# Kernel tuning notes

Hardware: AMD Instinct MI355X
Metric: run time of the kernel (lower is better)

The kernel has to match this reference:

```python
import jax, jax.numpy as jnp
import numpy as np
import math

B, C, H, W = 16, 512, 32, 32
HEADS = 8
HD = C // HEADS            # 64 head_dim
NFREQ = HD // 4            # 16 (head_dim % 4 == 0)
MAX_FREQ = 128.0
T = H * W                  # 1024 tokens


def _make_so2_mat():
    # make_2dcoord: meshgrid('ij') of arange(H), arange(W) -> [H, W, 2]
    xg, yg = np.meshgrid(np.arange(H, dtype=np.float32), np.arange(W, dtype=np.float32), indexing='ij')
    coord = np.stack([xg, yg], -1)                                   # [H, W, 2]
    freqs = np.exp(np.linspace(0.0, math.log(MAX_FREQ), NFREQ)).astype(np.float32)  # [NFREQ]
    th = coord[..., None, :] * freqs[None, None, :, None]            # [H, W, NFREQ, 2]
    c, s = np.cos(th), np.sin(th)
    # rotation matrices [[c, -s], [s, c]] -> [H, W, NFREQ, 2(dim), 2, 2]
    mat = np.stack([np.stack([c, -s], -1), np.stack([s, c], -1)], -2)
    mat = mat.reshape(H * W, NFREQ * 2, 2, 2)                        # flatten(2,3) then flatten(0,1)
    return jnp.asarray(mat[:, : HD // 2])                            # [T, HD//2, 2, 2]


def setup_inputs() -> dict:
    key = jax.random.key(0)
    ks = jax.random.split(key, 5)
    mat = _make_so2_mat()
    return {
        'x': jax.random.normal(ks[0], (B, C, H, W), dtype=jnp.float32),
        'w_qkv': jax.random.normal(ks[1], (3 * C, C), dtype=jnp.float32) * 0.02,
        'b_qkv': jax.random.normal(ks[2], (3 * C,), dtype=jnp.float32) * 0.02,
        'w_o': jax.random.normal(ks[3], (C, C), dtype=jnp.float32) * 0.02,
        'b_o': jax.random.normal(ks[4], (C,), dtype=jnp.float32) * 0.02,
        'mat_q': mat,
        'mat_k': mat,
        'mat_v': mat,
        'mat_o': jnp.swapaxes(mat, -2, -1),
    }


def _rep_mul(rep, t):
    # rep: [T, HD//2, 2, 2]; t: [B, nh, T, HD] -> per-pair 2x2 rotation
    tb = t.reshape(B, HEADS, T, HD // 2, 2)
    return jnp.einsum('tfij,bntfj->bntfi', rep, tb).reshape(B, HEADS, T, HD)


def _split_heads(t):
    # 'b (c nh) h w -> b nh (h w) c' (c outer, nh inner in channel dim)
    return t.reshape(B, HD, HEADS, T).transpose(0, 2, 3, 1)


def reference(x, w_qkv, b_qkv, w_o, b_o, mat_q, mat_k, mat_v, mat_o):
    # 1x1 conv QKV projection == channel GEMM
    qkv = jnp.einsum('bchw,oc->bohw', x, w_qkv) + b_qkv[None, :, None, None]
    q, k, v = jnp.split(qkv, 3, axis=1)
    q, k, v = map(_split_heads, (q, k, v))                 # [B, nh, T, HD]
    q = _rep_mul(mat_q, q)
    k = _rep_mul(mat_k, k)
    v = _rep_mul(mat_v, v)
    scale = 1.0 / math.sqrt(HD)
    attn = jax.nn.softmax(jnp.einsum('bntd,bnsd->bnts', q, k) * scale, axis=-1)
    o = jnp.einsum('bnts,bnsd->bntd', attn, v)             # [B, nh, T, HD]
    o = _rep_mul(mat_o, o)
    # 'b nh (h w) c -> b (c nh) h w'
    o = o.reshape(B, HEADS, H, W, HD).transpose(0, 4, 1, 2, 3).reshape(B, C, H, W)
    return jnp.einsum('bchw,oc->bohw', o, w_o) + b_o[None, :, None, None]
```

## Files before the change

### kernel.cpp

```cpp
#include <hip/hip_runtime.h>


typedef __bf16 bf16x8 __attribute__((ext_vector_type(8)));
typedef __bf16 bf16x4 __attribute__((ext_vector_type(4)));
typedef float  f32x4  __attribute__((ext_vector_type(4)));

__device__ __forceinline__ f32x4 mfma16(bf16x8 a, bf16x8 b, f32x4 c) {
    return __builtin_amdgcn_mfma_f32_16x16x32_bf16(a, b, c, 0, 0, 0);
}

__device__ __forceinline__ void async16(const void* g, void* l) {
    __builtin_amdgcn_global_load_lds(
        (const __attribute__((address_space(1))) void*)g,
        (__attribute__((address_space(3))) void*)l, 16, 0, 0);
}

__global__ void k_convert_w(const float* __restrict__ wq, const float* __restrict__ wo,
                            __bf16* __restrict__ wqb, __bf16* __restrict__ wob) {
    int i = blockIdx.x * 256 + threadIdx.x;
    if (i < 3 * 512 * 512) wqb[i] = (__bf16)wq[i];
    if (i < 512 * 512) {
        int o = i >> 9, k2 = i & 511;
        int nh = k2 >> 6, hd = k2 & 63;
        wob[i] = (__bf16)wo[o * 512 + hd * 8 + nh];
    }
}

__global__ void k_transpose_x(const float* __restrict__ x, __bf16* __restrict__ xt) {
    __shared__ float tile[32][33];
    const int b  = blockIdx.z;
    const int c0 = blockIdx.y * 32;
    const int t0 = blockIdx.x * 32;
    const int tx = threadIdx.x, ty = threadIdx.y;
    const float* xp = x + ((size_t)b * 512 + c0) * 1024 + t0;
#pragma unroll
    for (int j = 0; j < 4; j++)
        tile[ty + j * 8][tx] = xp[(ty + j * 8) * 1024 + tx];
    __syncthreads();
    __bf16* xo = xt + ((size_t)b * 1024 + t0) * 512 + c0;
#pragma unroll
    for (int j = 0; j < 4; j++)
        xo[(ty + j * 8) * 512 + tx] = (__bf16)tile[tx][ty + j * 8];
}

__global__ __launch_bounds__(256) void k_gemm_qkv(
        const __bf16* __restrict__ A, const __bf16* __restrict__ W,
        const float* __restrict__ bias,
        const float* __restrict__ matq, const float* __restrict__ matk,
        const float* __restrict__ matv,
        __bf16* __restrict__ qd, __bf16* __restrict__ kd, __bf16* __restrict__ vtd)
{
    __shared__ __bf16 As[128][64];
    __shared__ __bf16 Bs[128][64];
    const int tid = threadIdx.x;
    const int m0 = blockIdx.x * 128;
    const int jb = blockIdx.y;
    const int part = jb >> 2;
    const int nh_base = (jb & 3) * 2;
    const int lane = tid & 63, w = tid >> 6;
    const int ln = lane & 15, quad = lane >> 4;
    const int wr = w >> 1, wc = w & 1;

    const int srow = lane >> 3;
    const int scol = (((lane & 7) ^ srow) * 8);

    const __bf16* arow[4];
    const __bf16* brow[4];
#pragma unroll
    for (int jj = 0; jj < 4; jj++) {
        int rr = w * 32 + jj * 8 + srow;
        arow[jj] = &A[(size_t)(m0 + rr) * 512 + scol];
        int o = part * 512 + (rr & 63) * 8 + nh_base + (rr >> 6);
        brow[jj] = &W[(size_t)o * 512 + scol];
    }

    f32x4 acc[4][4] = {};

    for (int k0 = 0; k0 < 512; k0 += 64) {
#pragma unroll
        for (int jj = 0; jj < 4; jj++)
            async16(arow[jj] + k0, &As[w * 32 + jj * 8][0]);
#pragma unroll
        for (int jj = 0; jj < 4; jj++)
            async16(brow[jj] + k0, &Bs[w * 32 + jj * 8][0]);
        __syncthreads();
#pragma unroll
        for (int h = 0; h < 2; h++) {
            bf16x8 af[4], wf[4];
#pragma unroll
            for (int mi = 0; mi < 4; mi++)
                af[mi] = *(const bf16x8*)&As[wr * 64 + mi * 16 + ln][(((h * 4 + quad) ^ (ln & 7)) * 8)];
#pragma unroll
            for (int ni = 0; ni < 4; ni++)
                wf[ni] = *(const bf16x8*)&Bs[wc * 64 + ni * 16 + ln][(((h * 4 + quad) ^ (ln & 7)) * 8)];
#pragma unroll
            for (int mi = 0; mi < 4; mi++)
#pragma unroll
                for (int ni = 0; ni < 4; ni++)
                    acc[mi][ni] = mfma16(af[mi], wf[ni], acc[mi][ni]);
        }
        __syncthreads();
    }

    const int nh = nh_base + wc;
    const int rowbase = m0 + wr * 64;
    const int b  = rowbase >> 10, t0 = rowbase & 1023;
    const int bh = b * 8 + nh;
    const int ip = ln & 1;
    const float2* matp = (const float2*)(part == 0 ? matq : (part == 1 ? matk : matv));
    __bf16* qkdst = (part == 0) ? qd : kd;

#pragma unroll
    for (int ni = 0; ni < 4; ni++) {
        const int hd = ni * 16 + ln;
        const int f  = hd >> 1;
        const float bias_o = bias[part * 512 + hd * 8 + nh];
#pragma unroll
        for (int mi = 0; mi < 4; mi++) {
            const int tq = t0 + mi * 16 + quad * 4;
            if (part < 2) {
#pragma unroll
                for (int r = 0; r < 4; r++) {
                    int t = tq + r;
                    float val = acc[mi][ni][r] + bias_o;
                    float pr  = __shfl_xor(val, 1);
                    float2 mv = matp[((size_t)t * 32 + f) * 2 + ip];
                    float e  = ip ? pr : val;
                    float oo = ip ? val : pr;
                    float rv = mv.x * e + mv.y * oo;
                    qkdst[((size_t)bh * 1024 + t) * 64 + hd] = (__bf16)rv;
                }
            } else {
                __bf16 pack[4];
#pragma unroll
                for (int r = 0; r < 4; r++) {
                    int t = tq + r;
                    float val = acc[mi][ni][r] + bias_o;
                    float pr  = __shfl_xor(val, 1);
                    float2 mv = matp[((size_t)t * 32 + f) * 2 + ip];
                    float e  = ip ? pr : val;
                    float oo = ip ? val : pr;
                    pack[r] = (__bf16)(mv.x * e + mv.y * oo);
                }
                *(uint2*)&vtd[((size_t)bh * 64 + hd) * 1024 + tq] = *(const uint2*)pack;
            }
        }
    }
}

__global__ __launch_bounds__(256) void k_attn(
        const __bf16* __restrict__ q, const __bf16* __restrict__ kk,
        const __bf16* __restrict__ vt, const float* __restrict__ mato,
        __bf16* __restrict__ od)
{
    __shared__ __bf16 Ks[64][64];
    __shared__ __bf16 Vs[64][64];
    __shared__ __bf16 Ps[4][32][64];
    const int bh = blockIdx.x, qt = blockIdx.y;
    const int tid = threadIdx.x, w = tid >> 6, lane = tid & 63;
    const int ln = lane & 15, quad = lane >> 4;
    const int lx = ln & 7;
    const int srow = lane >> 3;
    const int scol = ((lane & 7) ^ srow) * 8;
    const int qr0 = qt * 128 + w * 32;

    bf16x8 qa[2][2];
#pragma unroll
    for (int mi = 0; mi < 2; mi++)
#pragma unroll
        for (int ki = 0; ki < 2; ki++)
            qa[mi][ki] = *(const bf16x8*)&q[((size_t)bh * 1024 + qr0 + mi * 16 + ln) * 64 + ki * 32 + quad * 8];

    const __bf16* kbase = kk + (size_t)bh * 1024 * 64;
    const __bf16* vbase = vt + (size_t)bh * 64 * 1024;

    f32x4 oacc[2][4] = {};
    f32x4 lacc[2] = {};
    const float C_EXP = 0.18033688011112042f;

    bf16x8 ones;
#pragma unroll
    for (int j = 0; j < 8; j++) ones[j] = (__bf16)1.0f;

    for (int st = 0; st < 16; st++) {
#pragma unroll
        for (int i = 0; i < 2; i++) {
            int r0 = w * 16 + i * 8;
            async16(kbase + (size_t)(st * 64 + r0 + srow) * 64 + scol, &Ks[r0][0]);
            async16(vbase + (size_t)(r0 + srow) * 1024 + st * 64 + scol, &Vs[r0][0]);
        }
        __syncthreads();

#pragma unroll
        for (int si = 0; si < 4; si++) {
            bf16x8 kb0 = *(const bf16x8*)&Ks[si * 16 + ln][((quad    ) ^ lx) * 8];
            bf16x8 kb1 = *(const bf16x8*)&Ks[si * 16 + ln][((quad + 4) ^ lx) * 8];
            f32x4 sc[2] = {};
#pragma unroll
            for (int mi = 0; mi < 2; mi++) {
                sc[mi] = mfma16(kb0, qa[mi][0], sc[mi]);
                sc[mi] = mfma16(kb1, qa[mi][1], sc[mi]);
            }
#pragma unroll
            for (int mi = 0; mi < 2; mi++) {
                bf16x4 pk;
#pragma unroll
                for (int r = 0; r < 4; r++)
                    pk[r] = (__bf16)exp2f(sc[mi][r] * C_EXP);
                *(bf16x4*)((char*)&Ps[w][mi * 16 + ln][0]
                           + (((si * 2 + (quad >> 1)) ^ lx) * 16) + (quad & 1) * 8) = pk;
            }
        }

#pragma unroll
        for (int kt = 0; kt < 2; kt++) {
            bf16x8 pa[2];
#pragma unroll
            for (int mi = 0; mi < 2; mi++)
                pa[mi] = *(const bf16x8*)&Ps[w][mi * 16 + ln][((kt * 4 + quad) ^ lx) * 8];
#pragma unroll
            for (int ni = 0; ni < 4; ni++) {
                bf16x8 vb = *(const bf16x8*)&Vs[ni * 16 + ln][((kt * 4 + quad) ^ lx) * 8];
                oacc[0][ni] = mfma16(vb, pa[0], oacc[0][ni]);
                oacc[1][ni] = mfma16(vb, pa[1], oacc[1][ni]);
            }
            lacc[0] = mfma16(ones, pa[0], lacc[0]);
            lacc[1] = mfma16(ones, pa[1], lacc[1]);
        }
        __syncthreads();
    }

    const float4* mo4 = (const float4*)mato;
#pragma unroll
    for (int mi = 0; mi < 2; mi++) {
        const int t = qr0 + mi * 16 + ln;
        const float invl = 1.0f / lacc[mi][0];
#pragma unroll
        for (int ni = 0; ni < 4; ni++) {
            const int hd0 = ni * 16 + quad * 4;
            const int f   = hd0 >> 1;
            float v0 = oacc[mi][ni][0] * invl;
            float v1 = oacc[mi][ni][1] * invl;
            float v2 = oacc[mi][ni][2] * invl;
            float v3 = oacc[mi][ni][3] * invl;
            float4 m1 = mo4[(size_t)t * 32 + f];
            float4 m2 = mo4[(size_t)t * 32 + f + 1];
            __bf16 pk[4];
            pk[0] = (__bf16)(m1.x * v0 + m1.y * v1);
            pk[1] = (__bf16)(m1.z * v0 + m1.w * v1);
            pk[2] = (__bf16)(m2.x * v2 + m2.y * v3);
            pk[3] = (__bf16)(m2.z * v2 + m2.w * v3);
            *(uint2*)&od[((size_t)bh * 1024 + t) * 64 + hd0] = *(const uint2*)pk;
        }
    }
}

__global__ __launch_bounds__(256) void k_gemm_out(
        const __bf16* __restrict__ A, const __bf16* __restrict__ W,
        const float* __restrict__ bias, float* __restrict__ out)
{
    __shared__ __bf16 As[128][64];
    __shared__ __bf16 Bs[128][64];
    const int tid = threadIdx.x;
    const int m0 = blockIdx.x * 128;
    const int n0 = blockIdx.y * 128;
    const int lane = tid & 63, w = tid >> 6;
    const int ln = lane & 15, quad = lane >> 4;
    const int wr = w >> 1, wc = w & 1;

    const int srow = lane >> 3;
    const int scol = (((lane & 7) ^ srow) * 8);

    const int bb = m0 >> 10, t00 = m0 & 1023;

    const __bf16* arow[4];
    const __bf16* brow[4];
#pragma unroll
    for (int jj = 0; jj < 4; jj++) {
        int rr = w * 32 + jj * 8 + srow;
        arow[jj] = &A[((size_t)bb * 8192 + t00 + rr) * 64 + scol];
        brow[jj] = &W[(size_t)(n0 + rr) * 512 + scol];
    }

    f32x4 acc[4][4] = {};

    for (int k0 = 0; k0 < 512; k0 += 64) {
#pragma unroll
        for (int jj = 0; jj < 4; jj++)
            async16(arow[jj] + (size_t)k0 * 1024, &As[w * 32 + jj * 8][0]);
#pragma unroll
        for (int jj = 0; jj < 4; jj++)
            async16(brow[jj] + k0, &Bs[w * 32 + jj * 8][0]);
        __syncthreads();
#pragma unroll
        for (int h = 0; h < 2; h++) {
            bf16x8 af[4], wf[4];
#pragma unroll
            for (int mi = 0; mi < 4; mi++)
                af[mi] = *(const bf16x8*)&As[wr * 64 + mi * 16 + ln][(((h * 4 + quad) ^ (ln & 7)) * 8)];
#pragma unroll
            for (int ni = 0; ni < 4; ni++)
                wf[ni] = *(const bf16x8*)&Bs[wc * 64 + ni * 16 + ln][(((h * 4 + quad) ^ (ln & 7)) * 8)];
#pragma unroll
            for (int mi = 0; mi < 4; mi++)
#pragma unroll
                for (int ni = 0; ni < 4; ni++)
                    acc[mi][ni] = mfma16(af[mi], wf[ni], acc[mi][ni]);
        }
        __syncthreads();
    }

    const int rowbase = m0 + wr * 64;
    const int bb2 = rowbase >> 10, t0 = rowbase & 1023;
#pragma unroll
    for (int ni = 0; ni < 4; ni++) {
        int o = n0 + wc * 64 + ni * 16 + ln;
        float bias_o = bias[o];
#pragma unroll
        for (int mi = 0; mi < 4; mi++) {
            int t = t0 + mi * 16 + quad * 4;
            f32x4 v = acc[mi][ni];
            v[0] += bias_o; v[1] += bias_o; v[2] += bias_o; v[3] += bias_o;
            *(f32x4*)&out[((size_t)bb2 * 512 + o) * 1024 + t] = v;
        }
    }
}

extern "C" void kernel_launch(void* const* d_in, const int* in_sizes, int n_in,
                              void* d_out, int out_size, void* d_ws, size_t ws_size,
                              hipStream_t stream) {
    (void)in_sizes; (void)n_in; (void)out_size; (void)ws_size;
    const float* x     = (const float*)d_in[0];
    const float* w_qkv = (const float*)d_in[1];
    const float* b_qkv = (const float*)d_in[2];
    const float* w_o   = (const float*)d_in[3];
    const float* b_o   = (const float*)d_in[4];
    const float* mat_q = (const float*)d_in[5];
    const float* mat_k = (const float*)d_in[6];
    const float* mat_v = (const float*)d_in[7];
    const float* mat_o = (const float*)d_in[8];
    float* out = (float*)d_out;

    char* p = (char*)d_ws;
    __bf16* wqb = (__bf16*)p;  p += (size_t)3 * 512 * 512 * 2;
    __bf16* wob = (__bf16*)p;  p += (size_t)512 * 512 * 2;
    char* xt_base = p;
    __bf16* xt  = (__bf16*)p;  p += (size_t)16384 * 512 * 2;
    __bf16* qd  = (__bf16*)p;  p += (size_t)128 * 1024 * 64 * 2;
    __bf16* kd  = (__bf16*)p;  p += (size_t)128 * 1024 * 64 * 2;
    __bf16* vtd = (__bf16*)p;  p += (size_t)128 * 64 * 1024 * 2;
    __bf16* od  = (__bf16*)xt_base;

    k_convert_w  <<<dim3(3072),       dim3(256),    0, stream>>>(w_qkv, w_o, wqb, wob);
    k_transpose_x<<<dim3(32, 16, 16), dim3(32, 8),  0, stream>>>(x, xt);
    k_gemm_qkv   <<<dim3(128, 12),    dim3(256),    0, stream>>>(xt, wqb, b_qkv, mat_q, mat_k, mat_v, qd, kd, vtd);
    k_attn       <<<dim3(128, 8),     dim3(256),    0, stream>>>(qd, kd, vtd, mat_o, od);
    k_gemm_out   <<<dim3(128, 4),     dim3(256),    0, stream>>>(od, wob, b_o, out);
}
```

Baseline: 240.8 us.

## Use 8 waves of 16 query rows in attention and prescale Q

The attention block now runs 512 threads. Each wave owns 16 query rows instead of 32, which halves per-wave accumulator and register use and spreads each K/V tile load across more waves. The softmax exponent scale (log2e/sqrt(d)) is folded into Q inside the QKV GEMM epilogue, removing a multiply per score. The trade-off is less K/V fragment reuse per wave and more LDS fragment reads per MFMA. Q is also rounded to bf16 after scaling, which slightly changes numerics.

```diff
diff --git a/kernel.cpp b/kernel.cpp
--- a/kernel.cpp
+++ b/kernel.cpp
@@ -109,6 +109,7 @@
     const int ip = ln & 1;
     const float2* matp = (const float2*)(part == 0 ? matq : (part == 1 ? matk : matv));
     __bf16* qkdst = (part == 0) ? qd : kd;
+    const float qscale = (part == 0) ? 0.18033688011112042f : 1.0f;
 
 #pragma unroll
     for (int ni = 0; ni < 4; ni++) {
@@ -127,7 +128,7 @@
                     float2 mv = matp[((size_t)t * 32 + f) * 2 + ip];
                     float e  = ip ? pr : val;
                     float oo = ip ? val : pr;
-                    float rv = mv.x * e + mv.y * oo;
+                    float rv = (mv.x * e + mv.y * oo) * qscale;
                     qkdst[((size_t)bh * 1024 + t) * 64 + hd] = (__bf16)rv;
                 }
             } else {
@@ -148,110 +149,89 @@
     }
 }
 
-__global__ __launch_bounds__(256) void k_attn(
+__global__ __launch_bounds__(512) void k_attn(
         const __bf16* __restrict__ q, const __bf16* __restrict__ kk,
         const __bf16* __restrict__ vt, const float* __restrict__ mato,
         __bf16* __restrict__ od)
 {
     __shared__ __bf16 Ks[64][64];
     __shared__ __bf16 Vs[64][64];
-    __shared__ __bf16 Ps[4][32][64];
+    __shared__ __bf16 Ps[8][16][64];
     const int bh = blockIdx.x, qt = blockIdx.y;
     const int tid = threadIdx.x, w = tid >> 6, lane = tid & 63;
     const int ln = lane & 15, quad = lane >> 4;
     const int lx = ln & 7;
     const int srow = lane >> 3;
     const int scol = ((lane & 7) ^ srow) * 8;
-    const int qr0 = qt * 128 + w * 32;
-
-    bf16x8 qa[2][2];
-#pragma unroll
-    for (int mi = 0; mi < 2; mi++)
-#pragma unroll
-        for (int ki = 0; ki < 2; ki++)
-            qa[mi][ki] = *(const bf16x8*)&q[((size_t)bh * 1024 + qr0 + mi * 16 + ln) * 64 + ki * 32 + quad * 8];
+    const int qr0 = qt * 128 + w * 16;
+
+    bf16x8 qa[2];
+#pragma unroll
+    for (int ki = 0; ki < 2; ki++)
+        qa[ki] = *(const bf16x8*)&q[((size_t)bh * 1024 + qr0 + ln) * 64 + ki * 32 + quad * 8];
 
     const __bf16* kbase = kk + (size_t)bh * 1024 * 64;
     const __bf16* vbase = vt + (size_t)bh * 64 * 1024;
 
-    f32x4 oacc[2][4] = {};
-    f32x4 lacc[2] = {};
-    const float C_EXP = 0.18033688011112042f;
+    f32x4 oacc[4] = {};
+    f32x4 lacc = {};
 
     bf16x8 ones;
 #pragma unroll
     for (int j = 0; j < 8; j++) ones[j] = (__bf16)1.0f;
 
     for (int st = 0; st < 16; st++) {
-#pragma unroll
-        for (int i = 0; i < 2; i++) {
-            int r0 = w * 16 + i * 8;
-            async16(kbase + (size_t)(st * 64 + r0 + srow) * 64 + scol, &Ks[r0][0]);
-            async16(vbase + (size_t)(r0 + srow) * 1024 + st * 64 + scol, &Vs[r0][0]);
-        }
+        async16(kbase + (size_t)(st * 64 + w * 8 + srow) * 64 + scol, &Ks[w * 8][0]);
+        async16(vbase + (size_t)(w * 8 + srow) * 1024 + st * 64 + scol, &Vs[w * 8][0]);
         __syncthreads();
 
 #pragma unroll
         for (int si = 0; si < 4; si++) {
             bf16x8 kb0 = *(const bf16x8*)&Ks[si * 16 + ln][((quad    ) ^ lx) * 8];
             bf16x8 kb1 = *(const bf16x8*)&Ks[si * 16 + ln][((quad + 4) ^ lx) * 8];
-            f32x4 sc[2] = {};
-#pragma unroll
-            for (int mi = 0; mi < 2; mi++) {
-                sc[mi] = mfma16(kb0, qa[mi][0], sc[mi]);
-                sc[mi] = mfma16(kb1, qa[mi][1], sc[mi]);
-            }
-#pragma unroll
-            for (int mi = 0; mi < 2; mi++) {
-                bf16x4 pk;
-#pragma unroll
-                for (int r = 0; r < 4; r++)
-                    pk[r] = (__bf16)exp2f(sc[mi][r] * C_EXP);
-                *(bf16x4*)((char*)&Ps[w][mi * 16 + ln][0]
-                           + (((si * 2 + (quad >> 1)) ^ lx) * 16) + (quad & 1) * 8) = pk;
-            }
+            f32x4 sc = {};
+            sc = mfma16(kb0, qa[0], sc);
+            sc = mfma16(kb1, qa[1], sc);
+            bf16x4 pk;
+#pragma unroll
+            for (int r = 0; r < 4; r++)
+                pk[r] = (__bf16)exp2f(sc[r]);
+            *(bf16x4*)((char*)&Ps[w][ln][0]
+                       + (((si * 2 + (quad >> 1)) ^ lx) * 16) + (quad & 1) * 8) = pk;
         }
 
 #pragma unroll
         for (int kt = 0; kt < 2; kt++) {
-            bf16x8 pa[2];
-#pragma unroll
-            for (int mi = 0; mi < 2; mi++)
-                pa[mi] = *(const bf16x8*)&Ps[w][mi * 16 + ln][((kt * 4 + quad) ^ lx) * 8];
+            bf16x8 pa = *(const bf16x8*)&Ps[w][ln][((kt * 4 + quad) ^ lx) * 8];
 #pragma unroll
             for (int ni = 0; ni < 4; ni++) {
                 bf16x8 vb = *(const bf16x8*)&Vs[ni * 16 + ln][((kt * 4 + quad) ^ lx) * 8];
-                oacc[0][ni] = mfma16(vb, pa[0], oacc[0][ni]);
-                oacc[1][ni] = mfma16(vb, pa[1], oacc[1][ni]);
+                oacc[ni] = mfma16(vb, pa, oacc[ni]);
             }
-            lacc[0] = mfma16(ones, pa[0], lacc[0]);
-            lacc[1] = mfma16(ones, pa[1], lacc[1]);
-        }
-        __syncthreads();
-    }
-
+            lacc = mfma16(ones, pa, lacc);
+        }
+        __syncthreads();
+    }
+
+    const float invl = 1.0f / lacc[0];
     const float4* mo4 = (const float4*)mato;
-#pragma unroll
-    for (int mi = 0; mi < 2; mi++) {
-        const int t = qr0 + mi * 16 + ln;
-        const float invl = 1.0f / lacc[mi][0];
-#pragma unroll
-        for (int ni = 0; ni < 4; ni++) {
-            const int hd0 = ni * 16 + quad * 4;
-            const int f   = hd0 >> 1;
-            float v0 = oacc[mi][ni][0] * invl;
-            float v1 = oacc[mi][ni][1] * invl;
-            float v2 = oacc[mi][ni][2] * invl;
-            float v3 = oacc[mi][ni][3] * invl;
-            float4 m1 = mo4[(size_t)t * 32 + f];
-            float4 m2 = mo4[(size_t)t * 32 + f + 1];
-            __bf16 pk[4];
-            pk[0] = (__bf16)(m1.x * v0 + m1.y * v1);
-            pk[1] = (__bf16)(m1.z * v0 + m1.w * v1);
-            pk[2] = (__bf16)(m2.x * v2 + m2.y * v3);
-            pk[3] = (__bf16)(m2.z * v2 + m2.w * v3);
-            *(uint2*)&od[((size_t)bh * 1024 + t) * 64 + hd0] = *(const uint2*)pk;
-        }
+    const int t = qr0 + ln;
+#pragma unroll
+    for (int ni = 0; ni < 4; ni++) {
+        const int hd0 = ni * 16 + quad * 4;
+        const int f   = hd0 >> 1;
+        float v0 = oacc[ni][0] * invl;
+        float v1 = oacc[ni][1] * invl;
+        float v2 = oacc[ni][2] * invl;
+        float v3 = oacc[ni][3] * invl;
+        float4 m1 = mo4[(size_t)t * 32 + f];
+        float4 m2 = mo4[(size_t)t * 32 + f + 1];
+        __bf16 pk[4];
+        pk[0] = (__bf16)(m1.x * v0 + m1.y * v1);
+        pk[1] = (__bf16)(m1.z * v0 + m1.w * v1);
+        pk[2] = (__bf16)(m2.x * v2 + m2.y * v3);
+        pk[3] = (__bf16)(m2.z * v2 + m2.w * v3);
+        *(uint2*)&od[((size_t)bh * 1024 + t) * 64 + hd0] = *(const uint2*)pk;
     }
 }
 
@@ -354,6 +334,6 @@
     k_convert_w  <<<dim3(3072),       dim3(256),    0, stream>>>(w_qkv, w_o, wqb, wob);
     k_transpose_x<<<dim3(32, 16, 16), dim3(32, 8),  0, stream>>>(x, xt);
     k_gemm_qkv   <<<dim3(128, 12),    dim3(256),    0, stream>>>(xt, wqb, b_qkv, mat_q, mat_k, mat_v, qd, kd, vtd);
-    k_attn       <<<dim3(128, 8),     dim3(256),    0, stream>>>(qd, kd, vtd, mat_o, od);
+    k_attn       <<<dim3(128, 8),     dim3(512),    0, stream>>>(qd, kd, vtd, mat_o, od);
     k_gemm_out   <<<dim3(128, 4),     dim3(256),    0, stream>>>(od, wob, b_o, out);
 }
```

Result: faster. 226.7 us (-5.9%).
